# Optimization experiments

Hardware: AMD Instinct MI355X
Metric: run time of the kernel (lower is better)

Reference implementation:

```python
import jax, jax.numpy as jnp
import numpy as np
from jax import lax

PAD_IDX = 0  # padding_index from init
B, T, E, H, V = 128, 24, 512, 512, 10000


def setup_inputs() -> dict:
    key = jax.random.key(0)
    ks = jax.random.split(key, 10)
    return {
        "images": jax.random.normal(ks[0], (B, H), jnp.float32),
        "captions": jax.random.randint(ks[1], (B, T), 0, V),
        "captions_length": jax.random.randint(ks[2], (B,), 1, T + 1),
        "W_emb": jax.random.normal(ks[3], (V, E), jnp.float32) * 0.02,
        "W_ih": jax.random.normal(ks[4], (4 * H, E), jnp.float32) * 0.02,
        "W_hh": jax.random.normal(ks[5], (4 * H, H), jnp.float32) * 0.02,
        "b_ih": jax.random.normal(ks[6], (4 * H,), jnp.float32) * 0.02,
        "b_hh": jax.random.normal(ks[7], (4 * H,), jnp.float32) * 0.02,
        "W_out": jax.random.normal(ks[8], (V, H), jnp.float32) * 0.02,
        "b_out": jax.random.normal(ks[9], (V,), jnp.float32) * 0.02,
    }


def reference(images, captions, captions_length, W_emb, W_ih, W_hh, b_ih, b_hh, W_out, b_out):
    # embedding with padding_idx: padding row forced to zero
    emb_table = W_emb.at[PAD_IDX].set(0.0)
    x = emb_table[captions]  # [B, T, E]
    bdim = images.shape[0]
    hdim = W_hh.shape[1]
    vocab = W_out.shape[0]
    bias = b_ih + b_hh

    def step(carry, xt):
        h, c = carry
        # PyTorch LSTMCell gate order: i, f, g, o
        gates = xt @ W_ih.T + h @ W_hh.T + bias  # [B, 4H]
        i, f, g, o = jnp.split(gates, 4, axis=-1)
        c = jax.nn.sigmoid(f) * c + jax.nn.sigmoid(i) * jnp.tanh(g)
        h = jax.nn.sigmoid(o) * jnp.tanh(c)
        logits = h @ W_out.T + b_out  # [B, V]
        return (h, c), logits

    c0 = jnp.zeros((bdim, hdim), images.dtype)
    _, ys = lax.scan(step, (images, c0), jnp.transpose(x, (1, 0, 2)))  # ys: [T, B, V]

    # deterministic <SOS>-like start output: one-hot at index 1, prepended at t=0
    start = jnp.zeros((vocab,), images.dtype).at[1].set(1.0)
    outputs = jnp.concatenate(
        [jnp.broadcast_to(start, (bdim, 1, vocab)), jnp.transpose(ys, (1, 0, 2))], axis=1
    )  # [B, T+1, V]
    return outputs, captions_length - 1
```

## Files before the change

kernel.cpp:

```cpp
#include <hip/hip_runtime.h>

constexpr int B_  = 128;
constexpr int T_  = 24;
constexpr int E_  = 512;
constexpr int H_  = 512;
constexpr int V_  = 10000;
constexpr int G4  = 2048;
constexpr int TP1 = 25;

typedef __attribute__((ext_vector_type(8))) short bf16x8;
typedef __attribute__((ext_vector_type(4))) short short4v;
typedef __attribute__((ext_vector_type(4))) float f32x4;

#define MFMA_16x16x32_BF16(a, b, c) __builtin_amdgcn_mfma_f32_16x16x32_bf16((a), (b), (c), 0, 0, 0)

__device__ inline unsigned short f2bf(float f) {
    unsigned int u = __float_as_uint(f);
    unsigned int r = (u + 0x7FFFu + ((u >> 16) & 1u)) >> 16;
    return (unsigned short)r;
}

__device__ inline void gl16(const unsigned short* g, unsigned short* l) {
    __builtin_amdgcn_global_load_lds(
        (const __attribute__((address_space(1))) unsigned int*)g,
        (__attribute__((address_space(3))) unsigned int*)l, 16, 0, 0);
}

__device__ inline int swz16(int row, int lq) {
    return (((row << 2) | lq) ^ (row & 7)) << 3;
}

__global__ __launch_bounds__(256) void k_prep(const float* __restrict__ Wih,
                                              const float* __restrict__ Whh,
                                              const float* __restrict__ Wout,
                                              const float* __restrict__ images,
                                              const float* __restrict__ Wemb,
                                              const int* __restrict__ captions,
                                              const int* __restrict__ cap_len,
                                              unsigned short* __restrict__ dWih,
                                              unsigned short* __restrict__ dWhh,
                                              unsigned short* __restrict__ dWout,
                                              unsigned short* __restrict__ dimg,
                                              unsigned short* __restrict__ Xemb,
                                              float* __restrict__ out,
                                              unsigned* __restrict__ flg,
                                              int do_start) {
    int b = blockIdx.x;
    if (b == 0) flg[threadIdx.x * 32] = 0u;
    if (b < 7112) {
        const float* src; unsigned short* dst; int i;
        if (b < 1024)      { src = Wih;    dst = dWih;  i = b * 256 + threadIdx.x; }
        else if (b < 2048) { src = Whh;    dst = dWhh;  i = (b - 1024) * 256 + threadIdx.x; }
        else if (b < 7048) { src = Wout;   dst = dWout; i = (b - 2048) * 256 + threadIdx.x; }
        else               { src = images; dst = dimg;  i = (b - 7048) * 256 + threadIdx.x; }
        float4 v = ((const float4*)src)[i];
        short4v o;
        o[0] = (short)f2bf(v.x); o[1] = (short)f2bf(v.y);
        o[2] = (short)f2bf(v.z); o[3] = (short)f2bf(v.w);
        ((short4v*)dst)[i] = o;
    } else if (b < 8648) {
        int i = (b - 7112) * 256 + threadIdx.x;
        int row = i >> 7;
        int k4  = i & 127;
        int bb = row & 127, t = row >> 7;
        int tok = captions[bb * T_ + t];
        short4v o = {0, 0, 0, 0};
        if (tok > 0 && tok < V_) {
            float4 v = ((const float4*)(Wemb + (long)tok * E_))[k4];
            o[0] = (short)f2bf(v.x); o[1] = (short)f2bf(v.y);
            o[2] = (short)f2bf(v.z); o[3] = (short)f2bf(v.w);
        }
        ((short4v*)Xemb)[(long)row * 128 + k4] = o;
    } else if (do_start) {
        int idx = (b - 8648) * 256 + threadIdx.x;
        constexpr int Q = V_ / 4;
        if (idx < B_ * Q) {
            int bb = idx / Q;
            int q = idx - bb * Q;
            float4 zero = {0.f, 0.f, 0.f, 0.f};
            float4 one1 = {0.f, 1.f, 0.f, 0.f};
            ((float4*)out)[(long)bb * (TP1 * Q) + q] = (q == 0) ? one1 : zero;
        }
        if (idx < B_)
            out[(size_t)B_ * TP1 * V_ + idx] = (float)(cap_len[idx] - 1);
    }
}

__global__ __launch_bounds__(256) void k_start(float* __restrict__ out,
                                               const int* __restrict__ cap_len) {
    int idx = blockIdx.x * 256 + threadIdx.x;
    constexpr int Q = V_ / 4;
    if (idx < B_ * Q) {
        int b = idx / Q;
        int q = idx - b * Q;
        float4 zero = {0.f, 0.f, 0.f, 0.f};
        float4 one1 = {0.f, 1.f, 0.f, 0.f};
        ((float4*)out)[(long)b * (TP1 * Q) + q] = (q == 0) ? one1 : zero;
    }
    if (idx < B_) out[(size_t)B_ * TP1 * V_ + idx] = (float)(cap_len[idx] - 1);
}

__global__ __launch_bounds__(256) void k_pregemm(const unsigned short* __restrict__ Xemb,
                                                 const unsigned short* __restrict__ Wih,
                                                 const float* __restrict__ bih,
                                                 const float* __restrict__ bhh,
                                                 float* __restrict__ P) {
    __shared__ unsigned short ldsA[2][4096];
    __shared__ unsigned short ldsB[2][4096];
    int bid = blockIdx.x;
    int xcd = bid & 7;
    int q   = bid >> 3;
    int MI  = xcd * 3 + (q % 3);
    int NI  = q / 3;
    int i    = threadIdx.x;
    int w = i >> 6, lane = i & 63;
    int lm = lane & 15, lq = lane >> 4;
    int wr = w >> 1, wc = w & 1;

    int mm0 = ((i >> 2) & 7) ^ ((i >> 4) & 1);
    int li  = i ^ mm0;
    const unsigned short* gA = Xemb + (size_t)(MI * 128 + (li >> 2)) * 512 + (li & 3) * 8;
    const unsigned short* gB = Wih  + (size_t)(NI * 128 + (li >> 2)) * 512 + (li & 3) * 8;
    unsigned short* lA = &ldsA[0][0] + i * 8;
    unsigned short* lB = &ldsB[0][0] + i * 8;

    auto stage = [&](int buf, int ks) {
        int go = ks * 32;
        gl16(gA + go,            lA + buf * 4096);
        gl16(gA + go + 64 * 512, lA + buf * 4096 + 2048);
        gl16(gB + go,            lB + buf * 4096);
        gl16(gB + go + 64 * 512, lB + buf * 4096 + 2048);
    };

    f32x4 acc[4][4] = {};
    stage(0, 0);
    for (int ksi = 0; ksi < 16; ksi++) {
        int cur = ksi & 1;
        if (ksi < 15) stage(cur ^ 1, ksi + 1);
        __syncthreads();
        bf16x8 af[4], bfr[4];
        #pragma unroll
        for (int mi = 0; mi < 4; mi++)
            af[mi] = *(const bf16x8*)&ldsA[cur][swz16(wr * 64 + mi * 16 + lm, lq)];
        #pragma unroll
        for (int ni = 0; ni < 4; ni++)
            bfr[ni] = *(const bf16x8*)&ldsB[cur][swz16(wc * 64 + ni * 16 + lm, lq)];
        #pragma unroll
        for (int mi = 0; mi < 4; mi++)
            #pragma unroll
            for (int ni = 0; ni < 4; ni++)
                acc[mi][ni] = MFMA_16x16x32_BF16(af[mi], bfr[ni], acc[mi][ni]);
        __syncthreads();
    }

    float bias[4];
    #pragma unroll
    for (int ni = 0; ni < 4; ni++) {
        int n = NI * 128 + wc * 64 + ni * 16 + lm;
        bias[ni] = bih[n] + bhh[n];
    }
    #pragma unroll
    for (int mi = 0; mi < 4; mi++) {
        #pragma unroll
        for (int r = 0; r < 4; r++) {
            int m = MI * 128 + wr * 64 + mi * 16 + lq * 4 + r;
            #pragma unroll
            for (int ni = 0; ni < 4; ni++) {
                int n = NI * 128 + wc * 64 + ni * 16 + lm;
                P[(size_t)m * G4 + n] = acc[mi][ni][r] + bias[ni];
            }
        }
    }
}

__global__ __launch_bounds__(256, 1) void k_lstm(const float* __restrict__ P,
                                                 const unsigned short* __restrict__ h0,
                                                 unsigned* __restrict__ hx0,
                                                 unsigned* __restrict__ hx1,
                                                 unsigned short* __restrict__ Hall,
                                                 const unsigned short* __restrict__ Whh,
                                                 unsigned* __restrict__ flg) {
    __shared__ float part[16][4][64];
    int w    = threadIdx.x >> 6;
    int lane = threadIdx.x & 63;
    int lm = lane & 15, lq = lane >> 4;
    int MI = blockIdx.x >> 5;
    int HG = blockIdx.x & 31;
    int hcol = HG * 16 + lm;
    int ks = w * 128;
    int brow = MI * 16 + lq * 4 + w;
    unsigned* myFlg = flg + (MI * 32 + HG) * 32;
    unsigned* wFlg  = flg + (MI * 32 + (w << 3)) * 32;

    bf16x8 bw[4][4];
    #pragma unroll
    for (int g = 0; g < 4; g++)
        #pragma unroll
        for (int kk = 0; kk < 4; kk++)
            bw[g][kk] = *(const bf16x8*)((const short*)Whh +
                          (size_t)(g * 512 + hcol) * 512 + ks + kk * 32 + lq * 8);

    float cp = 0.f;

    for (int t = 0; t < T_; t++) {
        const float* Pr = P + (size_t)t * B_ * G4 + (size_t)brow * G4;
        float pv0 = Pr[0 * 512 + hcol];
        float pv1 = Pr[1 * 512 + hcol];
        float pv2 = Pr[2 * 512 + hcol];
        float pv3 = Pr[3 * 512 + hcol];

        bf16x8 a[4];
        if (t == 0) {
            const unsigned short* A = h0 + (size_t)(MI * 16 + lm) * 512 + ks;
            #pragma unroll
            for (int kk = 0; kk < 4; kk++)
                a[kk] = *(const bf16x8*)(A + kk * 32 + lq * 8);
        } else {
            if (lane < 8) {
                unsigned want = (unsigned)t;
                while (__hip_atomic_load(wFlg + lane * 32, __ATOMIC_RELAXED,
                                         __HIP_MEMORY_SCOPE_AGENT) < want)
                    __builtin_amdgcn_s_sleep(1);
            }
            __builtin_amdgcn_wave_barrier();
            asm volatile("" ::: "memory");
            const unsigned long long* A = (const unsigned long long*)
                (((t & 1) ? hx1 : hx0) + ((size_t)(MI * 16 + lm) * 512 + ks) / 2);
            #pragma unroll
            for (int kk = 0; kk < 4; kk++) {
                union { unsigned long long q[2]; bf16x8 v; } cv;
                cv.q[0] = __hip_atomic_load(A + kk * 8 + lq * 2,
                                            __ATOMIC_RELAXED, __HIP_MEMORY_SCOPE_AGENT);
                cv.q[1] = __hip_atomic_load(A + kk * 8 + lq * 2 + 1,
                                            __ATOMIC_RELAXED, __HIP_MEMORY_SCOPE_AGENT);
                a[kk] = cv.v;
            }
        }

        f32x4 acc[4] = {};
        #pragma unroll
        for (int kk = 0; kk < 4; kk++) {
            acc[0] = MFMA_16x16x32_BF16(a[kk], bw[0][kk], acc[0]);
            acc[1] = MFMA_16x16x32_BF16(a[kk], bw[1][kk], acc[1]);
            acc[2] = MFMA_16x16x32_BF16(a[kk], bw[2][kk], acc[2]);
            acc[3] = MFMA_16x16x32_BF16(a[kk], bw[3][kk], acc[3]);
        }

        #pragma unroll
        for (int g = 0; g < 4; g++)
            #pragma unroll
            for (int r = 0; r < 4; r++)
                part[g * 4 + r][w][lane] = acc[g][r];
        __syncthreads();

        float gi = part[0*4+w][0][lane] + part[0*4+w][1][lane] + part[0*4+w][2][lane] + part[0*4+w][3][lane] + pv0;
        float gf = part[1*4+w][0][lane] + part[1*4+w][1][lane] + part[1*4+w][2][lane] + part[1*4+w][3][lane] + pv1;
        float gg = part[2*4+w][0][lane] + part[2*4+w][1][lane] + part[2*4+w][2][lane] + part[2*4+w][3][lane] + pv2;
        float go = part[3*4+w][0][lane] + part[3*4+w][1][lane] + part[3*4+w][2][lane] + part[3*4+w][3][lane] + pv3;
        float si = 1.f / (1.f + expf(-gi));
        float sf = 1.f / (1.f + expf(-gf));
        float so = 1.f / (1.f + expf(-go));
        float cn = sf * cp + si * tanhf(gg);
        float hn = so * tanhf(cn);
        cp = cn;
        unsigned short hb = f2bf(hn);

        if (t < T_ - 1) {
            unsigned up = ((unsigned)(unsigned short)__shfl_down((int)hb, 1) << 16) | (unsigned)hb;
            unsigned* HW = (t & 1) ? hx0 : hx1;
            if (!(lm & 1))
                __hip_atomic_store(HW + (brow * 512 + hcol) / 2, up,
                                   __ATOMIC_RELAXED, __HIP_MEMORY_SCOPE_AGENT);
            asm volatile("s_waitcnt vmcnt(0)" ::: "memory");
            __syncthreads();
            if (threadIdx.x == 0)
                __hip_atomic_store(myFlg, (unsigned)(t + 1), __ATOMIC_RELAXED,
                                   __HIP_MEMORY_SCOPE_AGENT);
        }
        Hall[(size_t)t * (B_ * H_) + brow * 512 + hcol] = hb;
    }
}

__global__ __launch_bounds__(512) void k_logits(const unsigned short* __restrict__ Hall,
                                                const unsigned short* __restrict__ Wout,
                                                const float* __restrict__ bout,
                                                float* __restrict__ out) {
    __shared__ unsigned short ldsA[2][8192];
    __shared__ unsigned short ldsB[2][8192];
    int bid = blockIdx.x;
    int xcd = bid & 7;
    int q   = bid >> 3;
    int MI  = q % 12;
    int NI  = xcd * 5 + q / 12;
    int i    = threadIdx.x;
    int w = i >> 6, lane = i & 63;
    int lm = lane & 15, lq = lane >> 4;
    int wr = w >> 2, wc = w & 3;

    int mm0 = ((i >> 2) & 7) ^ ((i >> 4) & 1);
    int li  = i ^ mm0;
    const unsigned short* gA = Hall + (size_t)(MI * 256 + (li >> 2)) * 512 + (li & 3) * 8;
    const unsigned short* gB = Wout + (size_t)(NI * 256 + (li >> 2)) * 512 + (li & 3) * 8;
    unsigned short* lA = &ldsA[0][0] + i * 8;
    unsigned short* lB = &ldsB[0][0] + i * 8;

    auto stage = [&](int buf, int ks) {
        int go = ks * 32;
        gl16(gA + go,             lA + buf * 8192);
        gl16(gA + go + 128 * 512, lA + buf * 8192 + 4096);
        gl16(gB + go,             lB + buf * 8192);
        gl16(gB + go + 128 * 512, lB + buf * 8192 + 4096);
    };

    f32x4 acc[8][4] = {};
    stage(0, 0);
    for (int ksi = 0; ksi < 16; ksi++) {
        int cur = ksi & 1;
        if (ksi < 15) stage(cur ^ 1, ksi + 1);
        __syncthreads();
        bf16x8 af[8], bfr[4];
        #pragma unroll
        for (int mi = 0; mi < 8; mi++)
            af[mi] = *(const bf16x8*)&ldsA[cur][swz16(wr * 128 + mi * 16 + lm, lq)];
        #pragma unroll
        for (int ni = 0; ni < 4; ni++)
            bfr[ni] = *(const bf16x8*)&ldsB[cur][swz16(wc * 64 + ni * 16 + lm, lq)];
        #pragma unroll
        for (int mi = 0; mi < 8; mi++)
            #pragma unroll
            for (int ni = 0; ni < 4; ni++)
                acc[mi][ni] = MFMA_16x16x32_BF16(af[mi], bfr[ni], acc[mi][ni]);
        __syncthreads();
    }

    float bias[4];
    #pragma unroll
    for (int ni = 0; ni < 4; ni++) {
        int n = NI * 256 + wc * 64 + ni * 16 + lm;
        bias[ni] = (n < V_) ? bout[n] : 0.f;
    }

    #pragma unroll
    for (int mi = 0; mi < 8; mi++) {
        #pragma unroll
        for (int r = 0; r < 4; r++) {
            int m = MI * 256 + wr * 128 + mi * 16 + lq * 4 + r;
            int b = m & 127, t = m >> 7;
            float* orow = out + ((size_t)b * TP1 + t + 1) * V_;
            #pragma unroll
            for (int ni = 0; ni < 4; ni++) {
                int n = NI * 256 + wc * 64 + ni * 16 + lm;
                if (n < V_) orow[n] = acc[mi][ni][r] + bias[ni];
            }
        }
    }
}

extern "C" void kernel_launch(void* const* d_in, const int* in_sizes, int n_in,
                              void* d_out, int out_size, void* d_ws, size_t ws_size,
                              hipStream_t stream) {
    const float* images   = (const float*)d_in[0];
    const int*   captions = (const int*)d_in[1];
    const int*   cap_len  = (const int*)d_in[2];
    const float* Wemb     = (const float*)d_in[3];
    const float* Wih      = (const float*)d_in[4];
    const float* Whh      = (const float*)d_in[5];
    const float* bih      = (const float*)d_in[6];
    const float* bhh      = (const float*)d_in[7];
    const float* Wout     = (const float*)d_in[8];
    const float* bout     = (const float*)d_in[9];
    float* out = (float*)d_out;

    char* ws = (char*)d_ws;
    unsigned short* Wih_bf  = (unsigned short*)(ws);
    unsigned short* Whh_bf  = (unsigned short*)(ws + 2097152);
    unsigned short* Wout_bf = (unsigned short*)(ws + 4194304);
    unsigned short* Xemb    = (unsigned short*)(ws + 14680064);
    unsigned short* Hall    = (unsigned short*)(ws + 17825792);
    unsigned short* h0      = (unsigned short*)(ws + 20971520);
    unsigned*       hx0     = (unsigned*)(ws + 21102592);
    unsigned*       hx1     = (unsigned*)(ws + 21233664);
    unsigned*       flg     = (unsigned*)(ws + 21364736);
    constexpr size_t P_OFF   = 21397504;
    constexpr size_t WS_NEED = P_OFF + 25165824;
    bool ws_ok = (ws_size >= WS_NEED);
    float* P = ws_ok ? (float*)(ws + P_OFF) : (float*)d_out;

    k_prep<<<9898, 256, 0, stream>>>(Wih, Whh, Wout, images, Wemb, captions,
                                     cap_len, Wih_bf, Whh_bf, Wout_bf, h0,
                                     Xemb, out, flg, ws_ok ? 1 : 0);

    k_pregemm<<<384, 256, 0, stream>>>(Xemb, Wih_bf, bih, bhh, P);

    k_lstm<<<256, 256, 0, stream>>>(P, h0, hx0, hx1, Hall, Whh_bf, flg);

    if (!ws_ok) k_start<<<1250, 256, 0, stream>>>(out, cap_len);

    k_logits<<<480, 512, 0, stream>>>(Hall, Wout_bf, bout, out);
}
```

Measured before the change: 330.2 us.

## Fuse input projection into LSTM recurrence and retile logits GEMM

Drops the separate input-projection GEMM and its fp32 gate buffer P. Each LSTM step now computes x_t·W_ih with MFMA from W_ih fragments held in registers, plus the bias, alongside the recurrent product. This removes one launch and a large fp32 write and read, but adds MFMA work and per-step embedding loads to the latency-critical serial loop. The logits GEMM moves from 256x256 tiles with 512 threads to 128x128 tiles with 256 threads over many more blocks, and the start-token fallback path is removed.

```diff
diff --git a/kernel.cpp b/kernel.cpp
--- a/kernel.cpp
+++ b/kernel.cpp
@@ -43,8 +43,7 @@
                                               unsigned short* __restrict__ dimg,
                                               unsigned short* __restrict__ Xemb,
                                               float* __restrict__ out,
-                                              unsigned* __restrict__ flg,
-                                              int do_start) {
+                                              unsigned* __restrict__ flg) {
     int b = blockIdx.x;
     if (b == 0) flg[threadIdx.x * 32] = 0u;
     if (b < 7112) {
@@ -71,7 +70,7 @@
             o[2] = (short)f2bf(v.z); o[3] = (short)f2bf(v.w);
         }
         ((short4v*)Xemb)[(long)row * 128 + k4] = o;
-    } else if (do_start) {
+    } else {
         int idx = (b - 8648) * 256 + threadIdx.x;
         constexpr int Q = V_ / 4;
         if (idx < B_ * Q) {
@@ -86,99 +85,15 @@
     }
 }
 
-__global__ __launch_bounds__(256) void k_start(float* __restrict__ out,
-                                               const int* __restrict__ cap_len) {
-    int idx = blockIdx.x * 256 + threadIdx.x;
-    constexpr int Q = V_ / 4;
-    if (idx < B_ * Q) {
-        int b = idx / Q;
-        int q = idx - b * Q;
-        float4 zero = {0.f, 0.f, 0.f, 0.f};
-        float4 one1 = {0.f, 1.f, 0.f, 0.f};
-        ((float4*)out)[(long)b * (TP1 * Q) + q] = (q == 0) ? one1 : zero;
-    }
-    if (idx < B_) out[(size_t)B_ * TP1 * V_ + idx] = (float)(cap_len[idx] - 1);
-}
-
-__global__ __launch_bounds__(256) void k_pregemm(const unsigned short* __restrict__ Xemb,
-                                                 const unsigned short* __restrict__ Wih,
-                                                 const float* __restrict__ bih,
-                                                 const float* __restrict__ bhh,
-                                                 float* __restrict__ P) {
-    __shared__ unsigned short ldsA[2][4096];
-    __shared__ unsigned short ldsB[2][4096];
-    int bid = blockIdx.x;
-    int xcd = bid & 7;
-    int q   = bid >> 3;
-    int MI  = xcd * 3 + (q % 3);
-    int NI  = q / 3;
-    int i    = threadIdx.x;
-    int w = i >> 6, lane = i & 63;
-    int lm = lane & 15, lq = lane >> 4;
-    int wr = w >> 1, wc = w & 1;
-
-    int mm0 = ((i >> 2) & 7) ^ ((i >> 4) & 1);
-    int li  = i ^ mm0;
-    const unsigned short* gA = Xemb + (size_t)(MI * 128 + (li >> 2)) * 512 + (li & 3) * 8;
-    const unsigned short* gB = Wih  + (size_t)(NI * 128 + (li >> 2)) * 512 + (li & 3) * 8;
-    unsigned short* lA = &ldsA[0][0] + i * 8;
-    unsigned short* lB = &ldsB[0][0] + i * 8;
-
-    auto stage = [&](int buf, int ks) {
-        int go = ks * 32;
-        gl16(gA + go,            lA + buf * 4096);
-        gl16(gA + go + 64 * 512, lA + buf * 4096 + 2048);
-        gl16(gB + go,            lB + buf * 4096);
-        gl16(gB + go + 64 * 512, lB + buf * 4096 + 2048);
-    };
-
-    f32x4 acc[4][4] = {};
-    stage(0, 0);
-    for (int ksi = 0; ksi < 16; ksi++) {
-        int cur = ksi & 1;
-        if (ksi < 15) stage(cur ^ 1, ksi + 1);
-        __syncthreads();
-        bf16x8 af[4], bfr[4];
-        #pragma unroll
-        for (int mi = 0; mi < 4; mi++)
-            af[mi] = *(const bf16x8*)&ldsA[cur][swz16(wr * 64 + mi * 16 + lm, lq)];
-        #pragma unroll
-        for (int ni = 0; ni < 4; ni++)
-            bfr[ni] = *(const bf16x8*)&ldsB[cur][swz16(wc * 64 + ni * 16 + lm, lq)];
-        #pragma unroll
-        for (int mi = 0; mi < 4; mi++)
-            #pragma unroll
-            for (int ni = 0; ni < 4; ni++)
-                acc[mi][ni] = MFMA_16x16x32_BF16(af[mi], bfr[ni], acc[mi][ni]);
-        __syncthreads();
-    }
-
-    float bias[4];
-    #pragma unroll
-    for (int ni = 0; ni < 4; ni++) {
-        int n = NI * 128 + wc * 64 + ni * 16 + lm;
-        bias[ni] = bih[n] + bhh[n];
-    }
-    #pragma unroll
-    for (int mi = 0; mi < 4; mi++) {
-        #pragma unroll
-        for (int r = 0; r < 4; r++) {
-            int m = MI * 128 + wr * 64 + mi * 16 + lq * 4 + r;
-            #pragma unroll
-            for (int ni = 0; ni < 4; ni++) {
-                int n = NI * 128 + wc * 64 + ni * 16 + lm;
-                P[(size_t)m * G4 + n] = acc[mi][ni][r] + bias[ni];
-            }
-        }
-    }
-}
-
-__global__ __launch_bounds__(256, 1) void k_lstm(const float* __restrict__ P,
+__global__ __launch_bounds__(256, 1) void k_lstm(const unsigned short* __restrict__ Xemb,
                                                  const unsigned short* __restrict__ h0,
                                                  unsigned* __restrict__ hx0,
                                                  unsigned* __restrict__ hx1,
                                                  unsigned short* __restrict__ Hall,
                                                  const unsigned short* __restrict__ Whh,
+                                                 const unsigned short* __restrict__ Wih,
+                                                 const float* __restrict__ bih,
+                                                 const float* __restrict__ bhh,
                                                  unsigned* __restrict__ flg) {
     __shared__ float part[16][4][64];
     int w    = threadIdx.x >> 6;
@@ -193,21 +108,38 @@
     unsigned* wFlg  = flg + (MI * 32 + (w << 3)) * 32;
 
     bf16x8 bw[4][4];
+    bf16x8 wv[4][4];
     #pragma unroll
     for (int g = 0; g < 4; g++)
         #pragma unroll
+        for (int kk = 0; kk < 4; kk++) {
+            size_t off = (size_t)(g * 512 + hcol) * 512 + ks + kk * 32 + lq * 8;
+            bw[g][kk] = *(const bf16x8*)((const short*)Whh + off);
+            wv[g][kk] = *(const bf16x8*)((const short*)Wih + off);
+        }
+
+    float bs0 = bih[0 * 512 + hcol] + bhh[0 * 512 + hcol];
+    float bs1 = bih[1 * 512 + hcol] + bhh[1 * 512 + hcol];
+    float bs2 = bih[2 * 512 + hcol] + bhh[2 * 512 + hcol];
+    float bs3 = bih[3 * 512 + hcol] + bhh[3 * 512 + hcol];
+
+    float cp = 0.f;
+
+    for (int t = 0; t < T_; t++) {
+        const unsigned short* X = Xemb + ((size_t)(t * 128 + MI * 16 + lm)) * 512 + ks;
+        bf16x8 xa[4];
+        #pragma unroll
         for (int kk = 0; kk < 4; kk++)
-            bw[g][kk] = *(const bf16x8*)((const short*)Whh +
-                          (size_t)(g * 512 + hcol) * 512 + ks + kk * 32 + lq * 8);
-
-    float cp = 0.f;
-
-    for (int t = 0; t < T_; t++) {
-        const float* Pr = P + (size_t)t * B_ * G4 + (size_t)brow * G4;
-        float pv0 = Pr[0 * 512 + hcol];
-        float pv1 = Pr[1 * 512 + hcol];
-        float pv2 = Pr[2 * 512 + hcol];
-        float pv3 = Pr[3 * 512 + hcol];
+            xa[kk] = *(const bf16x8*)(X + kk * 32 + lq * 8);
+
+        f32x4 acc[4] = {};
+        #pragma unroll
+        for (int kk = 0; kk < 4; kk++) {
+            acc[0] = MFMA_16x16x32_BF16(xa[kk], wv[0][kk], acc[0]);
+            acc[1] = MFMA_16x16x32_BF16(xa[kk], wv[1][kk], acc[1]);
+            acc[2] = MFMA_16x16x32_BF16(xa[kk], wv[2][kk], acc[2]);
+            acc[3] = MFMA_16x16x32_BF16(xa[kk], wv[3][kk], acc[3]);
+        }
 
         bf16x8 a[4];
         if (t == 0) {
@@ -237,7 +169,6 @@
             }
         }
 
-        f32x4 acc[4] = {};
         #pragma unroll
         for (int kk = 0; kk < 4; kk++) {
             acc[0] = MFMA_16x16x32_BF16(a[kk], bw[0][kk], acc[0]);
@@ -253,10 +184,10 @@
                 part[g * 4 + r][w][lane] = acc[g][r];
         __syncthreads();
 
-        float gi = part[0*4+w][0][lane] + part[0*4+w][1][lane] + part[0*4+w][2][lane] + part[0*4+w][3][lane] + pv0;
-        float gf = part[1*4+w][0][lane] + part[1*4+w][1][lane] + part[1*4+w][2][lane] + part[1*4+w][3][lane] + pv1;
-        float gg = part[2*4+w][0][lane] + part[2*4+w][1][lane] + part[2*4+w][2][lane] + part[2*4+w][3][lane] + pv2;
-        float go = part[3*4+w][0][lane] + part[3*4+w][1][lane] + part[3*4+w][2][lane] + part[3*4+w][3][lane] + pv3;
+        float gi = part[0*4+w][0][lane] + part[0*4+w][1][lane] + part[0*4+w][2][lane] + part[0*4+w][3][lane] + bs0;
+        float gf = part[1*4+w][0][lane] + part[1*4+w][1][lane] + part[1*4+w][2][lane] + part[1*4+w][3][lane] + bs1;
+        float gg = part[2*4+w][0][lane] + part[2*4+w][1][lane] + part[2*4+w][2][lane] + part[2*4+w][3][lane] + bs2;
+        float go = part[3*4+w][0][lane] + part[3*4+w][1][lane] + part[3*4+w][2][lane] + part[3*4+w][3][lane] + bs3;
         float si = 1.f / (1.f + expf(-gi));
         float sf = 1.f / (1.f + expf(-gf));
         float so = 1.f / (1.f + expf(-go));
@@ -281,76 +212,68 @@
     }
 }
 
-__global__ __launch_bounds__(512) void k_logits(const unsigned short* __restrict__ Hall,
+__global__ __launch_bounds__(256) void k_logits(const unsigned short* __restrict__ Hall,
                                                 const unsigned short* __restrict__ Wout,
                                                 const float* __restrict__ bout,
                                                 float* __restrict__ out) {
-    __shared__ unsigned short ldsA[2][8192];
-    __shared__ unsigned short ldsB[2][8192];
+    __shared__ unsigned short ldsA[2][4096];
+    __shared__ unsigned short ldsB[2][4096];
     int bid = blockIdx.x;
     int xcd = bid & 7;
     int q   = bid >> 3;
-    int MI  = q % 12;
-    int NI  = xcd * 5 + q / 12;
+    int MI  = xcd * 3 + (q % 3);
+    int NI  = q / 3;
     int i    = threadIdx.x;
     int w = i >> 6, lane = i & 63;
     int lm = lane & 15, lq = lane >> 4;
-    int wr = w >> 2, wc = w & 3;
+    int wr = w >> 1, wc = w & 1;
 
     int mm0 = ((i >> 2) & 7) ^ ((i >> 4) & 1);
     int li  = i ^ mm0;
-    const unsigned short* gA = Hall + (size_t)(MI * 256 + (li >> 2)) * 512 + (li & 3) * 8;
-    const unsigned short* gB = Wout + (size_t)(NI * 256 + (li >> 2)) * 512 + (li & 3) * 8;
+    const unsigned short* gA = Hall + (size_t)(MI * 128 + (li >> 2)) * 512 + (li & 3) * 8;
+    const unsigned short* gB = Wout + (size_t)(NI * 128 + (li >> 2)) * 512 + (li & 3) * 8;
     unsigned short* lA = &ldsA[0][0] + i * 8;
     unsigned short* lB = &ldsB[0][0] + i * 8;
 
     auto stage = [&](int buf, int ks) {
         int go = ks * 32;
-        gl16(gA + go,             lA + buf * 8192);
-        gl16(gA + go + 128 * 512, lA + buf * 8192 + 4096);
-        gl16(gB + go,             lB + buf * 8192);
-        gl16(gB + go + 128 * 512, lB + buf * 8192 + 4096);
+        gl16(gA + go,            lA + buf * 4096);
+        gl16(gA + go + 64 * 512, lA + buf * 4096 + 2048);
+        gl16(gB + go,            lB + buf * 4096);
+        gl16(gB + go + 64 * 512, lB + buf * 4096 + 2048);
     };
 
-    f32x4 acc[8][4] = {};
+    f32x4 acc[4][4] = {};
     stage(0, 0);
     for (int ksi = 0; ksi < 16; ksi++) {
         int cur = ksi & 1;
         if (ksi < 15) stage(cur ^ 1, ksi + 1);
         __syncthreads();
-        bf16x8 af[8], bfr[4];
-        #pragma unroll
-        for (int mi = 0; mi < 8; mi++)
-            af[mi] = *(const bf16x8*)&ldsA[cur][swz16(wr * 128 + mi * 16 + lm, lq)];
+        bf16x8 af[4], bfr[4];
+        #pragma unroll
+        for (int mi = 0; mi < 4; mi++)
+            af[mi] = *(const bf16x8*)&ldsA[cur][swz16(wr * 64 + mi * 16 + lm, lq)];
         #pragma unroll
         for (int ni = 0; ni < 4; ni++)
             bfr[ni] = *(const bf16x8*)&ldsB[cur][swz16(wc * 64 + ni * 16 + lm, lq)];
         #pragma unroll
-        for (int mi = 0; mi < 8; mi++)
+        for (int mi = 0; mi < 4; mi++)
             #pragma unroll
             for (int ni = 0; ni < 4; ni++)
                 acc[mi][ni] = MFMA_16x16x32_BF16(af[mi], bfr[ni], acc[mi][ni]);
         __syncthreads();
     }
 
-    float bias[4];
     #pragma unroll
-    for (int ni = 0; ni < 4; ni++) {
-        int n = NI * 256 + wc * 64 + ni * 16 + lm;
-        bias[ni] = (n < V_) ? bout[n] : 0.f;
-    }
-
-    #pragma unroll
-    for (int mi = 0; mi < 8; mi++) {
+    for (int mi = 0; mi < 4; mi++) {
         #pragma unroll
         for (int r = 0; r < 4; r++) {
-            int m = MI * 256 + wr * 128 + mi * 16 + lq * 4 + r;
-            int b = m & 127, t = m >> 7;
-            float* orow = out + ((size_t)b * TP1 + t + 1) * V_;
+            int b = wr * 64 + mi * 16 + lq * 4 + r;
+            float* orow = out + ((size_t)b * TP1 + MI + 1) * V_;
             #pragma unroll
             for (int ni = 0; ni < 4; ni++) {
-                int n = NI * 256 + wc * 64 + ni * 16 + lm;
-                if (n < V_) orow[n] = acc[mi][ni][r] + bias[ni];
+                int n = NI * 128 + wc * 64 + ni * 16 + lm;
+                if (n < V_) orow[n] = acc[mi][ni][r] + bout[n];
             }
         }
     }
@@ -375,26 +298,19 @@
     unsigned short* Wih_bf  = (unsigned short*)(ws);
     unsigned short* Whh_bf  = (unsigned short*)(ws + 2097152);
     unsigned short* Wout_bf = (unsigned short*)(ws + 4194304);
-    unsigned short* Xemb    = (unsigned short*)(ws + 14680064);
-    unsigned short* Hall    = (unsigned short*)(ws + 17825792);
-    unsigned short* h0      = (unsigned short*)(ws + 20971520);
-    unsigned*       hx0     = (unsigned*)(ws + 21102592);
-    unsigned*       hx1     = (unsigned*)(ws + 21233664);
-    unsigned*       flg     = (unsigned*)(ws + 21364736);
-    constexpr size_t P_OFF   = 21397504;
-    constexpr size_t WS_NEED = P_OFF + 25165824;
-    bool ws_ok = (ws_size >= WS_NEED);
-    float* P = ws_ok ? (float*)(ws + P_OFF) : (float*)d_out;
+    unsigned short* Xemb    = (unsigned short*)(ws + 14434304);
+    unsigned short* Hall    = (unsigned short*)(ws + 17580032);
+    unsigned short* h0      = (unsigned short*)(ws + 20725760);
+    unsigned*       hx0     = (unsigned*)(ws + 20856832);
+    unsigned*       hx1     = (unsigned*)(ws + 20987904);
+    unsigned*       flg     = (unsigned*)(ws + 21118976);
 
     k_prep<<<9898, 256, 0, stream>>>(Wih, Whh, Wout, images, Wemb, captions,
                                      cap_len, Wih_bf, Whh_bf, Wout_bf, h0,
-                                     Xemb, out, flg, ws_ok ? 1 : 0);
-
-    k_pregemm<<<384, 256, 0, stream>>>(Xemb, Wih_bf, bih, bhh, P);
-
-    k_lstm<<<256, 256, 0, stream>>>(P, h0, hx0, hx1, Hall, Whh_bf, flg);
-
-    if (!ws_ok) k_start<<<1250, 256, 0, stream>>>(out, cap_len);
-
-    k_logits<<<480, 512, 0, stream>>>(Hall, Wout_bf, bout, out);
-}
+                                     Xemb, out, flg);
+
+    k_lstm<<<256, 256, 0, stream>>>(Xemb, h0, hx0, hx1, Hall, Whh_bf, Wih_bf,
+                                    bih, bhh, flg);
+
+    k_logits<<<1896, 256, 0, stream>>>(Hall, Wout_bf, bout, out);
+}
```

Result: faster. 319.2 us (-3.3%).
